# Kernel tuning notes

Hardware: AMD Instinct MI355X
Metric: run time of the kernel (lower is better)

## Reference

```python
import jax, jax.numpy as jnp
import numpy as np

H = 512      # hidden_size
R = 47       # response_size
TR = 2       # treat_size
B = 128
T = 512


def _uniform(key, shape, k):
    return jax.random.uniform(key, shape, jnp.float32, -k, k)


def setup_inputs() -> dict:
    key = jax.random.key(0)
    ks = jax.random.split(key, 20)
    kinit = 1.0 / np.sqrt(H)
    inp = {
        "x_r": jax.random.normal(ks[0], (B, T, R), jnp.float32),
        "x_t": jax.random.normal(ks[1], (B, T, TR), jnp.float32),
        # r_rnn: 2-layer LSTM, input size R+TR=49 (torch gate order i,f,g,o)
        "r_Wih0": _uniform(ks[2], (4 * H, R + TR), kinit),
        "r_Whh0": _uniform(ks[3], (4 * H, H), kinit),
        "r_b0": _uniform(ks[4], (4 * H,), kinit),  # b_ih + b_hh fused
        "r_Wih1": _uniform(ks[5], (4 * H, H), kinit),
        "r_Whh1": _uniform(ks[6], (4 * H, H), kinit),
        "r_b1": _uniform(ks[7], (4 * H,), kinit),
        # t_rnn: 2-layer LSTM, input size 2*R+TR=96
        "t_Wih0": _uniform(ks[8], (4 * H, 2 * R + TR), kinit),
        "t_Whh0": _uniform(ks[9], (4 * H, H), kinit),
        "t_b0": _uniform(ks[10], (4 * H,), kinit),
        "t_Wih1": _uniform(ks[11], (4 * H, H), kinit),
        "t_Whh1": _uniform(ks[12], (4 * H, H), kinit),
        "t_b1": _uniform(ks[13], (4 * H,), kinit),
        # output linears
        "Wr": _uniform(ks[14], (R, H), kinit),
        "br": _uniform(ks[15], (R,), kinit),
        "Wt": _uniform(ks[16], (TR, H), kinit),
        "bt": _uniform(ks[17], (TR,), kinit),
    }
    return inp


def _lstm_cell(x, h, c, Wih, Whh, b):
    gates = x @ Wih.T + h @ Whh.T + b          # [B, 4H]
    i, f, g, o = jnp.split(gates, 4, axis=-1)
    c = jax.nn.sigmoid(f) * c + jax.nn.sigmoid(i) * jnp.tanh(g)
    h = jax.nn.sigmoid(o) * jnp.tanh(c)
    return h, c


def reference(x_r, x_t, r_Wih0, r_Whh0, r_b0, r_Wih1, r_Whh1, r_b1,
              t_Wih0, t_Whh0, t_b0, t_Wih1, t_Whh1, t_b1, Wr, br, Wt, bt):
    b = x_r.shape[0]
    z = jnp.zeros((b, H), x_r.dtype)
    carry0 = (z, z, z, z, z, z, z, z)  # (h,c) for 2 layers of r_rnn and t_rnn

    def step(carry, rt):
        hr0, cr0, hr1, cr1, ht0, ct0, ht1, ct1 = carry
        r, t = rt
        r_input = jnp.concatenate([r, t], axis=-1)          # [B, 49]
        hr0, cr0 = _lstm_cell(r_input, hr0, cr0, r_Wih0, r_Whh0, r_b0)
        hr1, cr1 = _lstm_cell(hr0, hr1, cr1, r_Wih1, r_Whh1, r_b1)
        r_out = hr1 @ Wr.T + br                             # [B, 47]
        t_input = jnp.concatenate([r_input, r_out], axis=-1)  # [B, 96]
        ht0, ct0 = _lstm_cell(t_input, ht0, ct0, t_Wih0, t_Whh0, t_b0)
        ht1, ct1 = _lstm_cell(ht0, ht1, ct1, t_Wih1, t_Whh1, t_b1)
        t_out = ht1 @ Wt.T + bt                             # [B, 2]
        return (hr0, cr0, hr1, cr1, ht0, ct0, ht1, ct1), (r_out, t_out)

    xs = (jnp.swapaxes(x_r, 0, 1), jnp.swapaxes(x_t, 0, 1))  # time-major [T,B,.]
    _, (r_seq, t_seq) = jax.lax.scan(step, carry0, xs)
    # back to batch-first, like the module's final permute(1,0,2)
    return jnp.swapaxes(r_seq, 0, 1), jnp.swapaxes(t_seq, 0, 1)
```

## Files before the change

kernel.cpp:

```cpp
#include <hip/hip_runtime.h>


typedef _Float16 half_t;
typedef _Float16 half8 __attribute__((ext_vector_type(8)));
typedef float floatx4 __attribute__((ext_vector_type(4)));
typedef unsigned long long ull_t;

#define OFF_W0 0
#define OFF_W1 131072
#define OFF_W2 1179648
#define OFF_W3 2228224
#define OFF_W4 3276800
#define OFF_W5 3407872
#define OFF_W6 3538944
#define OFF_W7 4587520
#define OFF_W8 5636096
#define OFF_W9 6684672
#define OFF_W10 6709248
#define W_TOTAL 6717440
#define H_BASE  6717440
#define RO_BASE 7241728
#define HALF_TOTAL 7258112
#define STATE_BYTE_OFF (H_BASE * 2)
#define C_BYTE_OFF (HALF_TOTAL * 2)
#define BAR_BYTE_OFF 15564800
#define X16_BYTE_OFF (BAR_BYTE_OFF + 4096)
#define WS_NEED_X16 ((unsigned long long)X16_BYTE_OFF + 8388608ull)
#define STATE_BYTES (X16_BYTE_OFF - STATE_BYTE_OFF)

#define NBLK 256
#define TOUT_BASE (128 * 512 * 47)

__device__ __forceinline__ floatx4 mfma16(half8 a, half8 b, floatx4 c) {
  return __builtin_amdgcn_mfma_f32_16x16x32_f16(a, b, c, 0, 0, 0);
}
__device__ __forceinline__ float fast_sig(float x) {
  x = fminf(fmaxf(x, -30.f), 30.f);
  float e = __expf(-x);
  return __builtin_amdgcn_rcpf(1.f + e);
}
__device__ __forceinline__ float fast_tanh(float x) {
  x = fminf(fmaxf(x, -15.f), 15.f);
  float e = __expf(-2.f * x);
  return (1.f - e) * __builtin_amdgcn_rcpf(1.f + e);
}

template <int N>
__device__ __forceinline__ void coh_stage(half8 (&bb)[N], const half_t* p) {
#pragma unroll
  for (int ks = 0; ks < N; ++ks)
    asm volatile("global_load_dwordx4 %0, %1, off sc0 sc1"
                 : "=v"(bb[ks]) : "v"(p + ks * 32));
}
__device__ __forceinline__ void drain_vm() {
  asm volatile("s_waitcnt vmcnt(0)" ::: "memory");
  __builtin_amdgcn_sched_barrier(0);
}
__device__ __forceinline__ void store_h4_coh(half_t* p, half_t h0, half_t h1,
                                             half_t h2, half_t h3) {
  union { ull_t u; _Float16 h[4]; } x;
  x.h[0] = h0; x.h[1] = h1; x.h[2] = h2; x.h[3] = h3;
  __hip_atomic_store((ull_t*)p, x.u, __ATOMIC_RELAXED,
                     __HIP_MEMORY_SCOPE_AGENT);
}
template <int PACE>
__device__ __forceinline__ void poll_llc(const unsigned* p, unsigned target) {
  for (;;) {
    unsigned v;
    asm volatile("global_load_dword %0, %1, off sc0 sc1\ns_waitcnt vmcnt(0)"
                 : "=v"(v) : "v"(p));
    if (v >= target) return;
    __builtin_amdgcn_s_sleep(PACE);
  }
}

__device__ __forceinline__ void slab_issue(half8 (&tmp)[4],
                                           const half_t* __restrict__ src,
                                           int tid) {
#pragma unroll
  for (int j = 0; j < 4; ++j) {
    const int u = tid + j * 256;
    asm volatile("global_load_dwordx4 %0, %1, off sc0 sc1"
                 : "=v"(tmp[j]) : "v"(src + (u >> 6) * 512 + (u & 63) * 8));
  }
}
__device__ __forceinline__ void slab_write(char* base, const half8 (&tmp)[4],
                                           int tid) {
#pragma unroll
  for (int j = 0; j < 4; ++j) {
    const int u = tid + j * 256;
    const int row = u >> 6, seg = u & 63;
    *(half8*)(base + row * 1024 + ((seg * 16) ^ ((row & 7) << 4))) = tmp[j];
  }
}

template <int NT, int NSEG, int LDW>
__device__ __forceinline__ void gemm_lb(const half_t* __restrict__ W,
                                        const int* wrow, const char* ldsb,
                                        int lk, int q, int l15,
                                        floatx4 (&acc)[NT]) {
  const int bbase = l15 * 1024;
  const int bxor = (l15 & 7) << 4;
#pragma unroll
  for (int ks = 0; ks < NSEG; ++ks) {
    const int kb = ks * 32 + lk;
    half8 b = *(const half8*)(ldsb + bbase + ((q * 16 + ks * 64) ^ bxor));
#pragma unroll
    for (int n = 0; n < NT; ++n) {
      half8 a = *(const half8*)(W + (long)(wrow[n] + l15) * LDW + kb);
      acc[n] = mfma16(a, b, acc[n]);
    }
  }
}

template <int NT, int NSEG, int LDW>
__device__ __forceinline__ void gemm_regB(const half_t* __restrict__ W,
                                          const int* wrow,
                                          const half8 (&bb)[NSEG], int lk,
                                          int l15, floatx4 (&acc)[NT]) {
#pragma unroll
  for (int ks = 0; ks < NSEG; ++ks) {
    const int kb = ks * 32 + lk;
#pragma unroll
    for (int n = 0; n < NT; ++n) {
      half8 a = *(const half8*)(W + (long)(wrow[n] + l15) * LDW + kb);
      acc[n] = mfma16(a, bb[ks], acc[n]);
    }
  }
}

__device__ __forceinline__ void gemm_x16(const half_t* __restrict__ W,
                                         const int* wrow,
                                         const half_t* __restrict__ xb, int lk,
                                         int l15, floatx4 (&acc)[4]) {
#pragma unroll
  for (int ks = 0; ks < 2; ++ks) {
    const int kb = ks * 32 + lk;
    half8 b = *(const half8*)(xb + kb);
#pragma unroll
    for (int n = 0; n < 4; ++n) {
      half8 a = *(const half8*)(W + (long)(wrow[n] + l15) * 64 + kb);
      acc[n] = mfma16(a, b, acc[n]);
    }
  }
}
__device__ __forceinline__ void gemm_xf(const float* __restrict__ xr,
                                        const float* __restrict__ xt, int t,
                                        int batch, const half_t* __restrict__ W,
                                        const int* wrow, int lk, int l15,
                                        floatx4 (&acc)[4]) {
#pragma unroll
  for (int ks = 0; ks < 2; ++ks) {
    const int kb = ks * 32 + lk;
    half8 b;
    const long base = (long)batch * 512 + t;
#pragma unroll
    for (int j = 0; j < 8; ++j) {
      const int kk = kb + j;
      float f = 0.f;
      if (kk < 47) f = xr[base * 47 + kk];
      else if (kk < 49) f = xt[base * 2 + (kk - 47)];
      b[j] = (half_t)f;
    }
#pragma unroll
    for (int n = 0; n < 4; ++n) {
      half8 a = *(const half8*)(W + (long)(wrow[n] + l15) * 64 + kb);
      acc[n] = mfma16(a, b, acc[n]);
    }
  }
}

__device__ __forceinline__ void lstm_epi_reg(floatx4 (&acc)[4],
                                             const float* __restrict__ bias,
                                             floatx4& creg,
                                             half_t* __restrict__ hdst,
                                             int batch, int hcol0) {
  const floatx4 bI = *(const floatx4*)(bias + hcol0);
  const floatx4 bF = *(const floatx4*)(bias + 512 + hcol0);
  const floatx4 bG = *(const floatx4*)(bias + 1024 + hcol0);
  const floatx4 bO = *(const floatx4*)(bias + 1536 + hcol0);
  const int off = batch * 512 + hcol0;
  half_t hn[4];
#pragma unroll
  for (int r = 0; r < 4; ++r) {
    const float gi = acc[0][r] + bI[r];
    const float gf = acc[1][r] + bF[r];
    const float gg = acc[2][r] + bG[r];
    const float go = acc[3][r] + bO[r];
    creg[r] = fast_sig(gf) * creg[r] + fast_sig(gi) * fast_tanh(gg);
    hn[r] = (half_t)(fast_sig(go) * fast_tanh(creg[r]));
  }
  store_h4_coh(hdst + off, hn[0], hn[1], hn[2], hn[3]);
}

__global__ __launch_bounds__(256, 1) void adrnn_persist(
    const float* __restrict__ xr, const float* __restrict__ xt,
    const float* __restrict__ b_r0, const float* __restrict__ b_r1,
    const float* __restrict__ b_t0, const float* __restrict__ b_t1,
    const float* __restrict__ brv, const float* __restrict__ btv,
    half_t* __restrict__ w16, float* __restrict__ cbase,
    float* __restrict__ out, unsigned* bar, const half_t* __restrict__ x16,
    int use_x16) {
  __shared__ half8 lds_v[2048];
  char* lds0 = (char*)lds_v;
  char* lds1 = lds0 + 16384;

  const int bid = blockIdx.x;
  const int tid = threadIdx.x;
  const int lane = tid & 63;
  const int w = tid >> 6;
  const int l15 = lane & 15;
  const int q = lane >> 4;
  const int lk = q * 8;
  half_t* H = w16 + H_BASE;
  half_t* RO = w16 + RO_BASE;
#define HB(cell, p) (H + (((cell)*2 + (p)) << 16))

  const int stage = (bid & 7) >> 1;
  const int hgHi = bid & 1;
  const int rr = bid >> 3;
  const int hgLo = rr >> 3;
  const int bg = rr & 7;
  const int hg = hgHi * 4 + hgLo;
  const int c0w = hg * 64 + w * 16;
  const int b0 = bg * 16;
  const int batch = b0 + l15;
  const int hcol0 = c0w + q * 4;
  const int sd = (stage == 0) ? 0 : (stage == 1) ? 1 : (stage == 2) ? 3 : 4;
  int wrow[4] = {c0w, 512 + c0w, 1024 + c0w, 1536 + c0w};
  const int flat = (hg * 8 + bg) * 4 + w;
  const bool is_spare = (stage == 0 && hg < 2 && flat < 32);

  unsigned* larr = bar + (bid & 7) * 32;
  unsigned* garr = bar + 256;
  unsigned* lgen = bar + 288 + (bid & 7) * 32;

  floatx4 creg = {0.f, 0.f, 0.f, 0.f};

  for (int k = 0; k < 517; ++k) {
    const int par = k & 1, pq = par ^ 1;
    const int t = k - sd;
    const bool valid = (t >= 0 && t < 512);

    if (valid) {
      half8 s0[4], s1[4];
      if (stage == 0) {
        slab_issue(s0, HB(0, pq) + b0 * 512, tid);
        drain_vm();
        slab_write(lds0, s0, tid);
      } else if (stage == 1) {
        slab_issue(s0, HB(0, pq) + b0 * 512, tid);
        slab_issue(s1, HB(1, pq) + b0 * 512, tid);
        drain_vm();
        slab_write(lds0, s0, tid);
        slab_write(lds1, s1, tid);
      } else if (stage == 2) {
        slab_issue(s0, HB(2, pq) + b0 * 512, tid);
        drain_vm();
        slab_write(lds0, s0, tid);
      } else {
        slab_issue(s0, HB(2, pq) + b0 * 512, tid);
        slab_issue(s1, HB(3, pq) + b0 * 512, tid);
        drain_vm();
        slab_write(lds0, s0, tid);
        slab_write(lds1, s1, tid);
      }
    }
    __syncthreads();

    if (valid) {
      floatx4 acc[4] = {};
      if (stage == 0) {
        if (use_x16)
          gemm_x16(w16 + OFF_W0, wrow, x16 + (long)t * 8192 + batch * 64, lk, l15, acc);
        else
          gemm_xf(xr, xt, t, batch, w16 + OFF_W0, wrow, lk, l15, acc);
        gemm_lb<4, 16, 512>(w16 + OFF_W1, wrow, lds0, lk, q, l15, acc);
        lstm_epi_reg(acc, b_r0, creg, HB(0, par), batch, hcol0);
      } else if (stage == 1) {
        gemm_lb<4, 16, 512>(w16 + OFF_W2, wrow, lds0, lk, q, l15, acc);
        gemm_lb<4, 16, 512>(w16 + OFF_W3, wrow, lds1, lk, q, l15, acc);
        lstm_epi_reg(acc, b_r1, creg, HB(1, par), batch, hcol0);
      } else if (stage == 2) {
        half8 bro[2];
        coh_stage<2>(bro, RO + pq * 8192 + batch * 64 + lk);
        drain_vm();
        if (use_x16)
          gemm_x16(w16 + OFF_W4, wrow, x16 + (long)t * 8192 + batch * 64, lk, l15, acc);
        else
          gemm_xf(xr, xt, t, batch, w16 + OFF_W4, wrow, lk, l15, acc);
        gemm_regB<4, 2, 64>(w16 + OFF_W5, wrow, bro, lk, l15, acc);
        gemm_lb<4, 16, 512>(w16 + OFF_W6, wrow, lds0, lk, q, l15, acc);
        lstm_epi_reg(acc, b_t0, creg, HB(2, par), batch, hcol0);
      } else {
        gemm_lb<4, 16, 512>(w16 + OFF_W7, wrow, lds0, lk, q, l15, acc);
        gemm_lb<4, 16, 512>(w16 + OFF_W8, wrow, lds1, lk, q, l15, acc);
        lstm_epi_reg(acc, b_t1, creg, HB(3, par), batch, hcol0);
      }
    }

    if (is_spare) {
      if (flat < 24) {
        const int tr = k - 2;
        if (tr >= 0 && tr < 512) {
          const int n = flat >> 3, btl = flat & 7;
          const int rb = btl * 16 + l15;
          half8 bs[16];
          coh_stage<16>(bs, HB(1, pq) + rb * 512 + lk);
          drain_vm();
          int wr1[1] = {n * 16};
          floatx4 accr[1] = {};
          gemm_regB<1, 16, 512>(w16 + OFF_W9, wr1, bs, lk, l15, accr);
          const int wc0 = n * 16 + q * 4;
          half_t ro4[4];
#pragma unroll
          for (int r = 0; r < 4; ++r) {
            const int wc = wc0 + r;
            float v = 0.f;
            if (wc < 47) {
              v = accr[0][r] + brv[wc];
              out[((long)rb * 512 + tr) * 47 + wc] = v;
            }
            ro4[r] = (half_t)v;
          }
          store_h4_coh(RO + par * 8192 + rb * 64 + wc0, ro4[0], ro4[1], ro4[2], ro4[3]);
        }
      } else {
        const int tt = k - 5;
        if (tt >= 0 && tt < 512) {
          const int btl = flat - 24;
          const int rb = btl * 16 + l15;
          half8 bs[16];
          coh_stage<16>(bs, HB(3, pq) + rb * 512 + lk);
          drain_vm();
          int wt1[1] = {0};
          floatx4 accw[1] = {};
          gemm_regB<1, 16, 512>(w16 + OFF_W10, wt1, bs, lk, l15, accw);
          if (q == 0) {
#pragma unroll
            for (int r = 0; r < 2; ++r)
              out[TOUT_BASE + ((long)rb * 512 + tt) * 2 + r] = accw[0][r] + btv[r];
          }
        }
      }
    }

    asm volatile("s_waitcnt vmcnt(0)" ::: "memory");
    __syncthreads();
    if (tid == 0) {
      const unsigned ku = (unsigned)k + 1u;
      (void)__hip_atomic_fetch_add(larr, 1u, __ATOMIC_RELAXED,
                                   __HIP_MEMORY_SCOPE_AGENT);
      if (bid < 8) {
        poll_llc<1>(larr, 32u * ku);
        (void)__hip_atomic_fetch_add(garr, 1u, __ATOMIC_RELAXED,
                                     __HIP_MEMORY_SCOPE_AGENT);
        poll_llc<1>(garr, 8u * ku);
        (void)__hip_atomic_fetch_add(lgen, 1u, __ATOMIC_RELAXED,
                                     __HIP_MEMORY_SCOPE_AGENT);
      } else {
        poll_llc<3>(lgen, ku);
      }
    }
    __syncthreads();
    asm volatile("" ::: "memory");
  }
#undef HB
}

__global__ __launch_bounds__(256) void conv_w(
    const float* __restrict__ rWih0, const float* __restrict__ rWhh0,
    const float* __restrict__ rWih1, const float* __restrict__ rWhh1,
    const float* __restrict__ tWih0, const float* __restrict__ tWhh0,
    const float* __restrict__ tWih1, const float* __restrict__ tWhh1,
    const float* __restrict__ Wr, const float* __restrict__ Wt,
    half_t* __restrict__ w16) {
  const int idx = blockIdx.x * 256 + threadIdx.x;
  if (idx >= W_TOTAL) return;
  float v = 0.f;
  if (idx < OFF_W1) {
    int n = idx >> 6, kk = idx & 63;
    if (kk < 49) v = rWih0[n * 49 + kk];
  } else if (idx < OFF_W2) {
    int r = idx - OFF_W1; v = rWhh0[r];
  } else if (idx < OFF_W3) {
    int r = idx - OFF_W2; v = rWih1[r];
  } else if (idx < OFF_W4) {
    int r = idx - OFF_W3; v = rWhh1[r];
  } else if (idx < OFF_W5) {
    int r = idx - OFF_W4; int n = r >> 6, kk = r & 63;
    if (kk < 49) v = tWih0[n * 96 + kk];
  } else if (idx < OFF_W6) {
    int r = idx - OFF_W5; int n = r >> 6, kk = r & 63;
    if (kk < 47) v = tWih0[n * 96 + 49 + kk];
  } else if (idx < OFF_W7) {
    int r = idx - OFF_W6; v = tWhh0[r];
  } else if (idx < OFF_W8) {
    int r = idx - OFF_W7; v = tWih1[r];
  } else if (idx < OFF_W9) {
    int r = idx - OFF_W8; v = tWhh1[r];
  } else if (idx < OFF_W10) {
    int r = idx - OFF_W9; int n = r >> 9, kk = r & 511;
    if (n < 47) v = Wr[n * 512 + kk];
  } else {
    int r = idx - OFF_W10; int n = r >> 9, kk = r & 511;
    if (n < 2) v = Wt[n * 512 + kk];
  }
  w16[idx] = (half_t)v;
}

__global__ __launch_bounds__(256) void conv_x(const float* __restrict__ xr,
                                              const float* __restrict__ xt,
                                              half_t* __restrict__ x16) {
  const int idx = blockIdx.x * 256 + threadIdx.x;
  if (idx >= 512 * 128 * 64) return;
  const int kk = idx & 63;
  const int row = (idx >> 6) & 127;
  const int t = idx >> 13;
  float v = 0.f;
  if (kk < 47) v = xr[(row * 512 + t) * 47 + kk];
  else if (kk < 49) v = xt[(row * 512 + t) * 2 + (kk - 47)];
  x16[idx] = (half_t)v;
}

extern "C" void kernel_launch(void* const* d_in, const int* in_sizes, int n_in,
                              void* d_out, int out_size, void* d_ws,
                              size_t ws_size, hipStream_t stream) {
  const float* xr = (const float*)d_in[0];
  const float* xt = (const float*)d_in[1];
  const float* rWih0 = (const float*)d_in[2];
  const float* rWhh0 = (const float*)d_in[3];
  const float* r_b0 = (const float*)d_in[4];
  const float* rWih1 = (const float*)d_in[5];
  const float* rWhh1 = (const float*)d_in[6];
  const float* r_b1 = (const float*)d_in[7];
  const float* tWih0 = (const float*)d_in[8];
  const float* tWhh0 = (const float*)d_in[9];
  const float* t_b0 = (const float*)d_in[10];
  const float* tWih1 = (const float*)d_in[11];
  const float* tWhh1 = (const float*)d_in[12];
  const float* t_b1 = (const float*)d_in[13];
  const float* Wr = (const float*)d_in[14];
  const float* br = (const float*)d_in[15];
  const float* Wt = (const float*)d_in[16];
  const float* bt = (const float*)d_in[17];

  half_t* w16 = (half_t*)d_ws;
  float* cbase = (float*)((char*)d_ws + C_BYTE_OFF);
  unsigned* bar = (unsigned*)((char*)d_ws + BAR_BYTE_OFF);
  half_t* x16 = (half_t*)((char*)d_ws + X16_BYTE_OFF);
  float* out = (float*)d_out;
  int use_x16 = (ws_size >= WS_NEED_X16) ? 1 : 0;

  (void)hipMemsetAsync((char*)d_ws + STATE_BYTE_OFF, 0, STATE_BYTES, stream);

  conv_w<<<(W_TOTAL + 255) / 256, 256, 0, stream>>>(
      rWih0, rWhh0, rWih1, rWhh1, tWih0, tWhh0, tWih1, tWhh1, Wr, Wt, w16);
  if (use_x16)
    conv_x<<<(512 * 128 * 64) / 256, 256, 0, stream>>>(xr, xt, x16);

  adrnn_persist<<<NBLK, 256, 0, stream>>>(xr, xt, r_b0, r_b1, t_b0, t_b1, br,
                                          bt, w16, cbase, out, bar, x16,
                                          use_x16);
}
```

Baseline: 9.246 ms.

## Replace global grid barrier with per-stage producer/consumer counters and 4-slot buffers

Replaces the per-step two-level global barrier across all 256 blocks with point-to-point counters: each stage polls only the write counters of the stages it consumes and the read counters of its consumers, using 4-deep rotating hidden-state buffers so producers can run ahead. The r_out and t_out output projections move from dedicated spare warps into stage-1 and stage-3 blocks, reusing the hidden state already staged in LDS. The goal is to cut global synchronisation latency and let pipeline stages overlap. In exchange it adds more atomic polling per step, grows the workspace for the extra buffers, and is more complex to get right.

```diff
diff --git a/kernel.cpp b/kernel.cpp
--- a/kernel.cpp
+++ b/kernel.cpp
@@ -19,12 +19,11 @@
 #define OFF_W10 6709248
 #define W_TOTAL 6717440
 #define H_BASE  6717440
-#define RO_BASE 7241728
-#define HALF_TOTAL 7258112
+#define RO_BASE 7766016
+#define HALF_TOTAL 7798784
 #define STATE_BYTE_OFF (H_BASE * 2)
-#define C_BYTE_OFF (HALF_TOTAL * 2)
-#define BAR_BYTE_OFF 15564800
-#define X16_BYTE_OFF (BAR_BYTE_OFF + 4096)
+#define BAR_BYTE_OFF (HALF_TOTAL * 2)
+#define X16_BYTE_OFF (BAR_BYTE_OFF + 16384)
 #define WS_NEED_X16 ((unsigned long long)X16_BYTE_OFF + 8388608ull)
 #define STATE_BYTES (X16_BYTE_OFF - STATE_BYTE_OFF)
 
@@ -46,7 +45,7 @@
 }
 
 template <int N>
-__device__ __forceinline__ void coh_stage(half8 (&bb)[N], const half_t* p) {
+__device__ __forceinline__ void burst_g(half8 (&bb)[N], const half_t* p) {
 #pragma unroll
   for (int ks = 0; ks < N; ++ks)
     asm volatile("global_load_dwordx4 %0, %1, off sc0 sc1"
@@ -56,22 +55,21 @@
   asm volatile("s_waitcnt vmcnt(0)" ::: "memory");
   __builtin_amdgcn_sched_barrier(0);
 }
-__device__ __forceinline__ void store_h4_coh(half_t* p, half_t h0, half_t h1,
-                                             half_t h2, half_t h3) {
-  union { ull_t u; _Float16 h[4]; } x;
-  x.h[0] = h0; x.h[1] = h1; x.h[2] = h2; x.h[3] = h3;
-  __hip_atomic_store((ull_t*)p, x.u, __ATOMIC_RELAXED,
-                     __HIP_MEMORY_SCOPE_AGENT);
-}
-template <int PACE>
+__device__ __forceinline__ void store_h4_coh(half_t* p, ull_t v) {
+  __hip_atomic_store((ull_t*)p, v, __ATOMIC_RELAXED, __HIP_MEMORY_SCOPE_AGENT);
+}
 __device__ __forceinline__ void poll_llc(const unsigned* p, unsigned target) {
   for (;;) {
     unsigned v;
     asm volatile("global_load_dword %0, %1, off sc0 sc1\ns_waitcnt vmcnt(0)"
                  : "=v"(v) : "v"(p));
     if (v >= target) return;
-    __builtin_amdgcn_s_sleep(PACE);
-  }
+    __builtin_amdgcn_s_sleep(1);
+  }
+}
+__device__ __forceinline__ void cnt_add(unsigned* p) {
+  (void)__hip_atomic_fetch_add(p, 1u, __ATOMIC_RELAXED,
+                               __HIP_MEMORY_SCOPE_AGENT);
 }
 
 __device__ __forceinline__ void slab_issue(half8 (&tmp)[4],
@@ -112,7 +110,6 @@
     }
   }
 }
-
 template <int NT, int NSEG, int LDW>
 __device__ __forceinline__ void gemm_regB(const half_t* __restrict__ W,
                                           const int* wrow,
@@ -128,7 +125,6 @@
     }
   }
 }
-
 __device__ __forceinline__ void gemm_x16(const half_t* __restrict__ W,
                                          const int* wrow,
                                          const half_t* __restrict__ xb, int lk,
@@ -180,7 +176,7 @@
   const floatx4 bG = *(const floatx4*)(bias + 1024 + hcol0);
   const floatx4 bO = *(const floatx4*)(bias + 1536 + hcol0);
   const int off = batch * 512 + hcol0;
-  half_t hn[4];
+  union { ull_t u; _Float16 h[4]; } pk;
 #pragma unroll
   for (int r = 0; r < 4; ++r) {
     const float gi = acc[0][r] + bI[r];
@@ -188,9 +184,9 @@
     const float gg = acc[2][r] + bG[r];
     const float go = acc[3][r] + bO[r];
     creg[r] = fast_sig(gf) * creg[r] + fast_sig(gi) * fast_tanh(gg);
-    hn[r] = (half_t)(fast_sig(go) * fast_tanh(creg[r]));
-  }
-  store_h4_coh(hdst + off, hn[0], hn[1], hn[2], hn[3]);
+    pk.h[r] = (half_t)(fast_sig(go) * fast_tanh(creg[r]));
+  }
+  store_h4_coh(hdst + off, pk.u);
 }
 
 __global__ __launch_bounds__(256, 1) void adrnn_persist(
@@ -214,7 +210,7 @@
   const int lk = q * 8;
   half_t* H = w16 + H_BASE;
   half_t* RO = w16 + RO_BASE;
-#define HB(cell, p) (H + (((cell)*2 + (p)) << 16))
+#define HB(cell, s) (H + (((cell)*4 + (s)) << 16))
 
   const int stage = (bid & 7) >> 1;
   const int hgHi = bid & 1;
@@ -228,45 +224,88 @@
   const int hcol0 = c0w + q * 4;
   const int sd = (stage == 0) ? 0 : (stage == 1) ? 1 : (stage == 2) ? 3 : 4;
   int wrow[4] = {c0w, 512 + c0w, 1024 + c0w, 1536 + c0w};
-  const int flat = (hg * 8 + bg) * 4 + w;
-  const bool is_spare = (stage == 0 && hg < 2 && flat < 32);
-
-  unsigned* larr = bar + (bid & 7) * 32;
-  unsigned* garr = bar + 256;
-  unsigned* lgen = bar + 288 + (bid & 7) * 32;
+
+#define WRH(c, b) (bar + ((c)*8 + (b)) * 32)
+#define RDA(c, b) (bar + 1024 + ((c)*8 + (b)) * 32)
+#define RDB(c, b) (bar + 2048 + ((c)*8 + (b)) * 32)
+#define WRRO(b)   (bar + 3072 + (b)*32)
+#define RDRO(b)   (bar + 3328 + (b)*32)
 
   floatx4 creg = {0.f, 0.f, 0.f, 0.f};
 
   for (int k = 0; k < 517; ++k) {
-    const int par = k & 1, pq = par ^ 1;
+    const int rs = (k - 1) & 3;
+    const int wsl = k & 3;
     const int t = k - sd;
     const bool valid = (t >= 0 && t < 512);
-
-    if (valid) {
+    const unsigned ku = (unsigned)k;
+
+    if (tid == 0) {
+      if (k > 0) {
+        if (stage == 0) {
+          poll_llc(WRH(0, bg), 8u * ku);
+        } else if (stage == 1) {
+          poll_llc(WRH(0, bg), 8u * ku);
+          poll_llc(WRH(1, bg), 8u * ku);
+        } else if (stage == 2) {
+          poll_llc(WRH(2, bg), 8u * ku);
+          poll_llc(WRRO(bg), ku);
+        } else {
+          poll_llc(WRH(2, bg), 8u * ku);
+          poll_llc(WRH(3, bg), 8u * ku);
+        }
+      }
+      if (k >= 3) {
+        const unsigned kw = ku - 2u;
+        if (stage == 0) {
+          poll_llc(RDA(0, bg), 8u * kw);
+          poll_llc(RDB(0, bg), 8u * kw);
+        } else if (stage == 1) {
+          poll_llc(RDA(1, bg), 8u * kw);
+          if (hg == 0) poll_llc(RDRO(bg), 8u * kw);
+        } else if (stage == 2) {
+          poll_llc(RDA(2, bg), 8u * kw);
+          poll_llc(RDB(2, bg), 8u * kw);
+        } else {
+          poll_llc(RDA(3, bg), 8u * kw);
+        }
+      }
+    }
+    __syncthreads();
+
+    half8 bro[2];
+    {
       half8 s0[4], s1[4];
       if (stage == 0) {
-        slab_issue(s0, HB(0, pq) + b0 * 512, tid);
+        slab_issue(s0, HB(0, rs) + b0 * 512, tid);
         drain_vm();
         slab_write(lds0, s0, tid);
       } else if (stage == 1) {
-        slab_issue(s0, HB(0, pq) + b0 * 512, tid);
-        slab_issue(s1, HB(1, pq) + b0 * 512, tid);
+        slab_issue(s0, HB(0, rs) + b0 * 512, tid);
+        slab_issue(s1, HB(1, rs) + b0 * 512, tid);
         drain_vm();
         slab_write(lds0, s0, tid);
         slab_write(lds1, s1, tid);
       } else if (stage == 2) {
-        slab_issue(s0, HB(2, pq) + b0 * 512, tid);
+        slab_issue(s0, HB(2, rs) + b0 * 512, tid);
+        burst_g<2>(bro, RO + rs * 8192 + batch * 64 + lk);
         drain_vm();
         slab_write(lds0, s0, tid);
       } else {
-        slab_issue(s0, HB(2, pq) + b0 * 512, tid);
-        slab_issue(s1, HB(3, pq) + b0 * 512, tid);
+        slab_issue(s0, HB(2, rs) + b0 * 512, tid);
+        slab_issue(s1, HB(3, rs) + b0 * 512, tid);
         drain_vm();
         slab_write(lds0, s0, tid);
         slab_write(lds1, s1, tid);
       }
     }
     __syncthreads();
+    if (tid == 0) {
+      if (stage == 0) cnt_add(RDA(0, bg));
+      else if (stage == 1) { cnt_add(RDB(0, bg)); cnt_add(RDA(1, bg)); }
+      else if (stage == 2) { cnt_add(RDA(2, bg)); cnt_add(RDRO(bg)); }
+      else { cnt_add(RDB(2, bg)); cnt_add(RDA(3, bg)); }
+    }
 
     if (valid) {
       floatx4 acc[4] = {};
@@ -276,96 +315,76 @@
         else
           gemm_xf(xr, xt, t, batch, w16 + OFF_W0, wrow, lk, l15, acc);
         gemm_lb<4, 16, 512>(w16 + OFF_W1, wrow, lds0, lk, q, l15, acc);
-        lstm_epi_reg(acc, b_r0, creg, HB(0, par), batch, hcol0);
+        lstm_epi_reg(acc, b_r0, creg, HB(0, wsl), batch, hcol0);
       } else if (stage == 1) {
         gemm_lb<4, 16, 512>(w16 + OFF_W2, wrow, lds0, lk, q, l15, acc);
         gemm_lb<4, 16, 512>(w16 + OFF_W3, wrow, lds1, lk, q, l15, acc);
-        lstm_epi_reg(acc, b_r1, creg, HB(1, par), batch, hcol0);
+        lstm_epi_reg(acc, b_r1, creg, HB(1, wsl), batch, hcol0);
       } else if (stage == 2) {
-        half8 bro[2];
-        coh_stage<2>(bro, RO + pq * 8192 + batch * 64 + lk);
-        drain_vm();
         if (use_x16)
           gemm_x16(w16 + OFF_W4, wrow, x16 + (long)t * 8192 + batch * 64, lk, l15, acc);
         else
           gemm_xf(xr, xt, t, batch, w16 + OFF_W4, wrow, lk, l15, acc);
         gemm_regB<4, 2, 64>(w16 + OFF_W5, wrow, bro, lk, l15, acc);
         gemm_lb<4, 16, 512>(w16 + OFF_W6, wrow, lds0, lk, q, l15, acc);
-        lstm_epi_reg(acc, b_t0, creg, HB(2, par), batch, hcol0);
+        lstm_epi_reg(acc, b_t0, creg, HB(2, wsl), batch, hcol0);
       } else {
         gemm_lb<4, 16, 512>(w16 + OFF_W7, wrow, lds0, lk, q, l15, acc);
         gemm_lb<4, 16, 512>(w16 + OFF_W8, wrow, lds1, lk, q, l15, acc);
-        lstm_epi_reg(acc, b_t1, creg, HB(3, par), batch, hcol0);
-      }
-    }
-
-    if (is_spare) {
-      if (flat < 24) {
-        const int tr = k - 2;
-        if (tr >= 0 && tr < 512) {
-          const int n = flat >> 3, btl = flat & 7;
-          const int rb = btl * 16 + l15;
-          half8 bs[16];
-          coh_stage<16>(bs, HB(1, pq) + rb * 512 + lk);
-          drain_vm();
-          int wr1[1] = {n * 16};
-          floatx4 accr[1] = {};
-          gemm_regB<1, 16, 512>(w16 + OFF_W9, wr1, bs, lk, l15, accr);
-          const int wc0 = n * 16 + q * 4;
-          half_t ro4[4];
-#pragma unroll
-          for (int r = 0; r < 4; ++r) {
-            const int wc = wc0 + r;
-            float v = 0.f;
-            if (wc < 47) {
-              v = accr[0][r] + brv[wc];
-              out[((long)rb * 512 + tr) * 47 + wc] = v;
-            }
-            ro4[r] = (half_t)v;
+        lstm_epi_reg(acc, b_t1, creg, HB(3, wsl), batch, hcol0);
+      }
+    }
+
+    if (stage == 1 && hg == 0 && w < 3) {
+      const int tro = k - 2;
+      if (tro >= 0 && tro < 512) {
+        int wr1[1] = {w * 16};
+        floatx4 accr[1] = {};
+        gemm_lb<1, 16, 512>(w16 + OFF_W9, wr1, lds1, lk, q, l15, accr);
+        const int rb = b0 + l15;
+        const int wc0 = w * 16 + q * 4;
+        union { ull_t u2; _Float16 h[4]; } rp;
+#pragma unroll
+        for (int r = 0; r < 4; ++r) {
+          const int wc = wc0 + r;
+          float v = 0.f;
+          if (wc < 47) {
+            v = accr[0][r] + brv[wc];
+            out[((long)rb * 512 + tro) * 47 + wc] = v;
           }
-          store_h4_coh(RO + par * 8192 + rb * 64 + wc0, ro4[0], ro4[1], ro4[2], ro4[3]);
+          rp.h[r] = (half_t)v;
         }
-      } else {
-        const int tt = k - 5;
-        if (tt >= 0 && tt < 512) {
-          const int btl = flat - 24;
-          const int rb = btl * 16 + l15;
-          half8 bs[16];
-          coh_stage<16>(bs, HB(3, pq) + rb * 512 + lk);
-          drain_vm();
-          int wt1[1] = {0};
-          floatx4 accw[1] = {};
-          gemm_regB<1, 16, 512>(w16 + OFF_W10, wt1, bs, lk, l15, accw);
-          if (q == 0) {
-#pragma unroll
-            for (int r = 0; r < 2; ++r)
-              out[TOUT_BASE + ((long)rb * 512 + tt) * 2 + r] = accw[0][r] + btv[r];
-          }
+        store_h4_coh(RO + wsl * 8192 + rb * 64 + wc0, rp.u2);
+      }
+    }
+    if (stage == 3 && hg == 0 && w == 0) {
+      const int tto = k - 5;
+      if (tto >= 0 && tto < 512) {
+        int wt1[1] = {0};
+        floatx4 accw[1] = {};
+        gemm_lb<1, 16, 512>(w16 + OFF_W10, wt1, lds1, lk, q, l15, accw);
+        if (q == 0) {
+          const int rb = b0 + l15;
+#pragma unroll
+          for (int r = 0; r < 2; ++r)
+            out[TOUT_BASE + ((long)rb * 512 + tto) * 2 + r] = accw[0][r] + btv[r];
         }
       }
     }
 
-    asm volatile("s_waitcnt vmcnt(0)" ::: "memory");
+    drain_vm();
     __syncthreads();
     if (tid == 0) {
-      const unsigned ku = (unsigned)k + 1u;
-      (void)__hip_atomic_fetch_add(larr, 1u, __ATOMIC_RELAXED,
-                                   __HIP_MEMORY_SCOPE_AGENT);
-      if (bid < 8) {
-        poll_llc<1>(larr, 32u * ku);
-        (void)__hip_atomic_fetch_add(garr, 1u, __ATOMIC_RELAXED,
-                                     __HIP_MEMORY_SCOPE_AGENT);
-        poll_llc<1>(garr, 8u * ku);
-        (void)__hip_atomic_fetch_add(lgen, 1u, __ATOMIC_RELAXED,
-                                     __HIP_MEMORY_SCOPE_AGENT);
-      } else {
-        poll_llc<3>(lgen, ku);
-      }
-    }
-    __syncthreads();
-    asm volatile("" ::: "memory");
+      cnt_add(WRH(stage, bg));
+      if (stage == 1 && hg == 0) cnt_add(WRRO(bg));
+    }
   }
 #undef HB
+#undef WRH
+#undef RDA
+#undef RDB
+#undef WRRO
+#undef RDRO
 }
 
 __global__ __launch_bounds__(256) void conv_w(
@@ -446,7 +465,7 @@
   const float* bt = (const float*)d_in[17];
 
   half_t* w16 = (half_t*)d_ws;
-  float* cbase = (float*)((char*)d_ws + C_BYTE_OFF);
+  float* cbase = nullptr;
   unsigned* bar = (unsigned*)((char*)d_ws + BAR_BYTE_OFF);
   half_t* x16 = (half_t*)((char*)d_ws + X16_BYTE_OFF);
   float* out = (float*)d_out;
```

After: 10.20 ms. 10.3% more time.

## Split K across two wave groups per block and prefetch weight fragments

Applied to the files above, without the earlier changes.

Doubles the block to 512 threads and has each half of the waves compute half of the K reduction for the same gate tile, then reduces the partial accumulators through LDS before the LSTM epilogue. The gemm_lb loop also gets software prefetching of the next weight fragment. The aim is to shorten each recurrent step's serial MFMA chain and hide weight-load latency. In exchange it adds two extra __syncthreads and LDS traffic per step, and uses more registers per wave.

```diff
diff --git a/kernel.cpp b/kernel.cpp
--- a/kernel.cpp
+++ b/kernel.cpp
@@ -56,12 +56,8 @@
   asm volatile("s_waitcnt vmcnt(0)" ::: "memory");
   __builtin_amdgcn_sched_barrier(0);
 }
-__device__ __forceinline__ void store_h4_coh(half_t* p, half_t h0, half_t h1,
-                                             half_t h2, half_t h3) {
-  union { ull_t u; _Float16 h[4]; } x;
-  x.h[0] = h0; x.h[1] = h1; x.h[2] = h2; x.h[3] = h3;
-  __hip_atomic_store((ull_t*)p, x.u, __ATOMIC_RELAXED,
-                     __HIP_MEMORY_SCOPE_AGENT);
+__device__ __forceinline__ void store_h4_coh(half_t* p, ull_t v) {
+  __hip_atomic_store((ull_t*)p, v, __ATOMIC_RELAXED, __HIP_MEMORY_SCOPE_AGENT);
 }
 template <int PACE>
 __device__ __forceinline__ void poll_llc(const unsigned* p, unsigned target) {
@@ -74,21 +70,21 @@
   }
 }
 
-__device__ __forceinline__ void slab_issue(half8 (&tmp)[4],
-                                           const half_t* __restrict__ src,
-                                           int tid) {
-#pragma unroll
-  for (int j = 0; j < 4; ++j) {
-    const int u = tid + j * 256;
+__device__ __forceinline__ void slab_issue2(half8 (&tmp)[2],
+                                            const half_t* __restrict__ src,
+                                            int tid) {
+#pragma unroll
+  for (int j = 0; j < 2; ++j) {
+    const int u = tid + j * 512;
     asm volatile("global_load_dwordx4 %0, %1, off sc0 sc1"
                  : "=v"(tmp[j]) : "v"(src + (u >> 6) * 512 + (u & 63) * 8));
   }
 }
-__device__ __forceinline__ void slab_write(char* base, const half8 (&tmp)[4],
-                                           int tid) {
-#pragma unroll
-  for (int j = 0; j < 4; ++j) {
-    const int u = tid + j * 256;
+__device__ __forceinline__ void slab_write2(char* base, const half8 (&tmp)[2],
+                                            int tid) {
+#pragma unroll
+  for (int j = 0; j < 2; ++j) {
+    const int u = tid + j * 512;
     const int row = u >> 6, seg = u & 63;
     *(half8*)(base + row * 1024 + ((seg * 16) ^ ((row & 7) << 4))) = tmp[j];
   }
@@ -97,22 +93,42 @@
 template <int NT, int NSEG, int LDW>
 __device__ __forceinline__ void gemm_lb(const half_t* __restrict__ W,
                                         const int* wrow, const char* ldsb,
-                                        int lk, int q, int l15,
+                                        int ks0, int lk, int q, int l15,
                                         floatx4 (&acc)[NT]) {
   const int bbase = l15 * 1024;
   const int bxor = (l15 & 7) << 4;
-#pragma unroll
-  for (int ks = 0; ks < NSEG; ++ks) {
-    const int kb = ks * 32 + lk;
+  half8 a_cur[NT], a_nxt[NT];
+#pragma unroll
+  for (int n = 0; n < NT; ++n)
+    a_cur[n] = *(const half8*)(W + (long)(wrow[n] + l15) * LDW + ks0 * 32 + lk);
+#pragma unroll
+  for (int ksl = 0; ksl < NSEG; ++ksl) {
+    const int ks = ks0 + ksl;
+    if (ksl + 1 < NSEG) {
+      const int kb2 = (ks + 1) * 32 + lk;
+#pragma unroll
+      for (int n = 0; n < NT; ++n)
+        a_nxt[n] = *(const half8*)(W + (long)(wrow[n] + l15) * LDW + kb2);
+    }
     half8 b = *(const half8*)(ldsb + bbase + ((q * 16 + ks * 64) ^ bxor));
 #pragma unroll
-    for (int n = 0; n < NT; ++n) {
-      half8 a = *(const half8*)(W + (long)(wrow[n] + l15) * LDW + kb);
-      acc[n] = mfma16(a, b, acc[n]);
-    }
-  }
-}
-
+    for (int n = 0; n < NT; ++n) acc[n] = mfma16(a_cur[n], b, acc[n]);
+#pragma unroll
+    for (int n = 0; n < NT; ++n) a_cur[n] = a_nxt[n];
+  }
+}
+template <int NT>
+__device__ __forceinline__ void gemm_seg(const half_t* __restrict__ W,
+                                         const int* wrow, half8 b, int ks,
+                                         int LDW, int lk, int l15,
+                                         floatx4 (&acc)[NT]) {
+  const int kb = ks * 32 + lk;
+#pragma unroll
+  for (int n = 0; n < NT; ++n) {
+    half8 a = *(const half8*)(W + (long)(wrow[n] + l15) * LDW + kb);
+    acc[n] = mfma16(a, b, acc[n]);
+  }
+}
 template <int NT, int NSEG, int LDW>
 __device__ __forceinline__ void gemm_regB(const half_t* __restrict__ W,
                                           const int* wrow,
@@ -129,45 +145,21 @@
   }
 }
 
-__device__ __forceinline__ void gemm_x16(const half_t* __restrict__ W,
-                                         const int* wrow,
-                                         const half_t* __restrict__ xb, int lk,
-                                         int l15, floatx4 (&acc)[4]) {
-#pragma unroll
-  for (int ks = 0; ks < 2; ++ks) {
-    const int kb = ks * 32 + lk;
-    half8 b = *(const half8*)(xb + kb);
-#pragma unroll
-    for (int n = 0; n < 4; ++n) {
-      half8 a = *(const half8*)(W + (long)(wrow[n] + l15) * 64 + kb);
-      acc[n] = mfma16(a, b, acc[n]);
-    }
-  }
-}
-__device__ __forceinline__ void gemm_xf(const float* __restrict__ xr,
-                                        const float* __restrict__ xt, int t,
-                                        int batch, const half_t* __restrict__ W,
-                                        const int* wrow, int lk, int l15,
-                                        floatx4 (&acc)[4]) {
-#pragma unroll
-  for (int ks = 0; ks < 2; ++ks) {
-    const int kb = ks * 32 + lk;
-    half8 b;
-    const long base = (long)batch * 512 + t;
-#pragma unroll
-    for (int j = 0; j < 8; ++j) {
-      const int kk = kb + j;
-      float f = 0.f;
-      if (kk < 47) f = xr[base * 47 + kk];
-      else if (kk < 49) f = xt[base * 2 + (kk - 47)];
-      b[j] = (half_t)f;
-    }
-#pragma unroll
-    for (int n = 0; n < 4; ++n) {
-      half8 a = *(const half8*)(W + (long)(wrow[n] + l15) * 64 + kb);
-      acc[n] = mfma16(a, b, acc[n]);
-    }
-  }
+__device__ __forceinline__ half8 build_bx1(const float* __restrict__ xr,
+                                           const float* __restrict__ xt, int t,
+                                           int batch, int ks, int lk) {
+  half8 b;
+  const long base = (long)batch * 512 + t;
+  const int kb = ks * 32 + lk;
+#pragma unroll
+  for (int j = 0; j < 8; ++j) {
+    const int kk = kb + j;
+    float f = 0.f;
+    if (kk < 47) f = xr[base * 47 + kk];
+    else if (kk < 49) f = xt[base * 2 + (kk - 47)];
+    b[j] = (half_t)f;
+  }
+  return b;
 }
 
 __device__ __forceinline__ void lstm_epi_reg(floatx4 (&acc)[4],
@@ -180,7 +172,7 @@
   const floatx4 bG = *(const floatx4*)(bias + 1024 + hcol0);
   const floatx4 bO = *(const floatx4*)(bias + 1536 + hcol0);
   const int off = batch * 512 + hcol0;
-  half_t hn[4];
+  union { ull_t u; _Float16 h[4]; } pk;
 #pragma unroll
   for (int r = 0; r < 4; ++r) {
     const float gi = acc[0][r] + bI[r];
@@ -188,12 +180,12 @@
     const float gg = acc[2][r] + bG[r];
     const float go = acc[3][r] + bO[r];
     creg[r] = fast_sig(gf) * creg[r] + fast_sig(gi) * fast_tanh(gg);
-    hn[r] = (half_t)(fast_sig(go) * fast_tanh(creg[r]));
-  }
-  store_h4_coh(hdst + off, hn[0], hn[1], hn[2], hn[3]);
-}
-
-__global__ __launch_bounds__(256, 1) void adrnn_persist(
+    pk.h[r] = (half_t)(fast_sig(go) * fast_tanh(creg[r]));
+  }
+  store_h4_coh(hdst + off, pk.u);
+}
+
+__global__ __launch_bounds__(512, 1) void adrnn_persist(
     const float* __restrict__ xr, const float* __restrict__ xt,
     const float* __restrict__ b_r0, const float* __restrict__ b_r1,
     const float* __restrict__ b_t0, const float* __restrict__ b_t1,
@@ -208,7 +200,9 @@
   const int bid = blockIdx.x;
   const int tid = threadIdx.x;
   const int lane = tid & 63;
-  const int w = tid >> 6;
+  const int w8 = tid >> 6;
+  const int hw = w8 & 3;
+  const int kh = w8 >> 2;
   const int l15 = lane & 15;
   const int q = lane >> 4;
   const int lk = q * 8;
@@ -222,14 +216,15 @@
   const int hgLo = rr >> 3;
   const int bg = rr & 7;
   const int hg = hgHi * 4 + hgLo;
-  const int c0w = hg * 64 + w * 16;
+  const int c0w = hg * 64 + hw * 16;
   const int b0 = bg * 16;
   const int batch = b0 + l15;
   const int hcol0 = c0w + q * 4;
   const int sd = (stage == 0) ? 0 : (stage == 1) ? 1 : (stage == 2) ? 3 : 4;
   int wrow[4] = {c0w, 512 + c0w, 1024 + c0w, 1536 + c0w};
-  const int flat = (hg * 8 + bg) * 4 + w;
-  const bool is_spare = (stage == 0 && hg < 2 && flat < 32);
+  const int ks0 = kh * 8;
+  const int flat = (hg * 8 + bg) * 4 + hw;
+  const bool is_spare = (stage == 0 && hg < 2 && flat < 32 && kh == 0);
 
   unsigned* larr = bar + (bid & 7) * 32;
   unsigned* garr = bar + 256;
@@ -243,60 +238,78 @@
     const bool valid = (t >= 0 && t < 512);
 
     if (valid) {
-      half8 s0[4], s1[4];
+      half8 s0[2], s1[2];
       if (stage == 0) {
-        slab_issue(s0, HB(0, pq) + b0 * 512, tid);
+        slab_issue2(s0, HB(0, pq) + b0 * 512, tid);
         drain_vm();
-        slab_write(lds0, s0, tid);
+        slab_write2(lds0, s0, tid);
       } else if (stage == 1) {
-        slab_issue(s0, HB(0, pq) + b0 * 512, tid);
-        slab_issue(s1, HB(1, pq) + b0 * 512, tid);
+        slab_issue2(s0, HB(0, pq) + b0 * 512, tid);
+        slab_issue2(s1, HB(1, pq) + b0 * 512, tid);
         drain_vm();
-        slab_write(lds0, s0, tid);
-        slab_write(lds1, s1, tid);
+        slab_write2(lds0, s0, tid);
+        slab_write2(lds1, s1, tid);
       } else if (stage == 2) {
-        slab_issue(s0, HB(2, pq) + b0 * 512, tid);
+        slab_issue2(s0, HB(2, pq) + b0 * 512, tid);
         drain_vm();
-        slab_write(lds0, s0, tid);
+        slab_write2(lds0, s0, tid);
       } else {
-        slab_issue(s0, HB(2, pq) + b0 * 512, tid);
-        slab_issue(s1, HB(3, pq) + b0 * 512, tid);
+        slab_issue2(s0, HB(2, pq) + b0 * 512, tid);
+        slab_issue2(s1, HB(3, pq) + b0 * 512, tid);
         drain_vm();
-        slab_write(lds0, s0, tid);
-        slab_write(lds1, s1, tid);
+        slab_write2(lds0, s0, tid);
+        slab_write2(lds1, s1, tid);
       }
     }
     __syncthreads();
 
+    floatx4 acc[4] = {};
     if (valid) {
-      floatx4 acc[4] = {};
       if (stage == 0) {
+        half8 bx;
         if (use_x16)
-          gemm_x16(w16 + OFF_W0, wrow, x16 + (long)t * 8192 + batch * 64, lk, l15, acc);
+          bx = *(const half8*)(x16 + (long)t * 8192 + batch * 64 + kh * 32 + lk);
         else
-          gemm_xf(xr, xt, t, batch, w16 + OFF_W0, wrow, lk, l15, acc);
-        gemm_lb<4, 16, 512>(w16 + OFF_W1, wrow, lds0, lk, q, l15, acc);
-        lstm_epi_reg(acc, b_r0, creg, HB(0, par), batch, hcol0);
+          bx = build_bx1(xr, xt, t, batch, kh, lk);
+        gemm_seg<4>(w16 + OFF_W0, wrow, bx, kh, 64, lk, l15, acc);
+        gemm_lb<4, 8, 512>(w16 + OFF_W1, wrow, lds0, ks0, lk, q, l15, acc);
       } else if (stage == 1) {
-        gemm_lb<4, 16, 512>(w16 + OFF_W2, wrow, lds0, lk, q, l15, acc);
-        gemm_lb<4, 16, 512>(w16 + OFF_W3, wrow, lds1, lk, q, l15, acc);
-        lstm_epi_reg(acc, b_r1, creg, HB(1, par), batch, hcol0);
+        gemm_lb<4, 8, 512>(w16 + OFF_W2, wrow, lds0, ks0, lk, q, l15, acc);
+        gemm_lb<4, 8, 512>(w16 + OFF_W3, wrow, lds1, ks0, lk, q, l15, acc);
       } else if (stage == 2) {
-        half8 bro[2];
-        coh_stage<2>(bro, RO + pq * 8192 + batch * 64 + lk);
+        half8 bro;
+        asm volatile("global_load_dwordx4 %0, %1, off sc0 sc1"
+                     : "=v"(bro)
+                     : "v"(RO + pq * 8192 + batch * 64 + kh * 32 + lk));
+        half8 bx;
+        if (use_x16)
+          bx = *(const half8*)(x16 + (long)t * 8192 + batch * 64 + kh * 32 + lk);
+        else
+          bx = build_bx1(xr, xt, t, batch, kh, lk);
+        gemm_seg<4>(w16 + OFF_W4, wrow, bx, kh, 64, lk, l15, acc);
         drain_vm();
-        if (use_x16)
-          gemm_x16(w16 + OFF_W4, wrow, x16 + (long)t * 8192 + batch * 64, lk, l15, acc);
-        else
-          gemm_xf(xr, xt, t, batch, w16 + OFF_W4, wrow, lk, l15, acc);
-        gemm_regB<4, 2, 64>(w16 + OFF_W5, wrow, bro, lk, l15, acc);
-        gemm_lb<4, 16, 512>(w16 + OFF_W6, wrow, lds0, lk, q, l15, acc);
-        lstm_epi_reg(acc, b_t0, creg, HB(2, par), batch, hcol0);
+        gemm_seg<4>(w16 + OFF_W5, wrow, bro, kh, 64, lk, l15, acc);
+        gemm_lb<4, 8, 512>(w16 + OFF_W6, wrow, lds0, ks0, lk, q, l15, acc);
       } else {
-        gemm_lb<4, 16, 512>(w16 + OFF_W7, wrow, lds0, lk, q, l15, acc);
-        gemm_lb<4, 16, 512>(w16 + OFF_W8, wrow, lds1, lk, q, l15, acc);
-        lstm_epi_reg(acc, b_t1, creg, HB(3, par), batch, hcol0);
+        gemm_lb<4, 8, 512>(w16 + OFF_W7, wrow, lds0, ks0, lk, q, l15, acc);
+        gemm_lb<4, 8, 512>(w16 + OFF_W8, wrow, lds1, ks0, lk, q, l15, acc);
       }
+    }
+    __syncthreads();
+
+    if (valid && kh == 1) {
+#pragma unroll
+      for (int n = 0; n < 4; ++n)
+        *(floatx4*)(lds0 + hw * 4096 + lane * 64 + n * 16) = acc[n];
+    }
+    __syncthreads();
+    if (valid && kh == 0) {
+#pragma unroll
+      for (int n = 0; n < 4; ++n)
+        acc[n] += *(const floatx4*)(lds0 + hw * 4096 + lane * 64 + n * 16);
+      const float* bias = (stage == 0) ? b_r0 : (stage == 1) ? b_r1
+                         : (stage == 2) ? b_t0 : b_t1;
+      lstm_epi_reg(acc, bias, creg, HB(stage, par), batch, hcol0);
     }
 
     if (is_spare) {
@@ -312,7 +325,7 @@
           floatx4 accr[1] = {};
           gemm_regB<1, 16, 512>(w16 + OFF_W9, wr1, bs, lk, l15, accr);
           const int wc0 = n * 16 + q * 4;
-          half_t ro4[4];
+          union { ull_t u2; _Float16 h[4]; } rp;
 #pragma unroll
           for (int r = 0; r < 4; ++r) {
             const int wc = wc0 + r;
@@ -321,9 +334,9 @@
               v = accr[0][r] + brv[wc];
               out[((long)rb * 512 + tr) * 47 + wc] = v;
             }
-            ro4[r] = (half_t)v;
+            rp.h[r] = (half_t)v;
           }
-          store_h4_coh(RO + par * 8192 + rb * 64 + wc0, ro4[0], ro4[1], ro4[2], ro4[3]);
+          store_h4_coh(RO + par * 8192 + rb * 64 + wc0, rp.u2);
         }
       } else {
         const int tt = k - 5;
@@ -446,7 +459,7 @@
   const float* bt = (const float*)d_in[17];
 
   half_t* w16 = (half_t*)d_ws;
-  float* cbase = (float*)((char*)d_ws + C_BYTE_OFF);
+  float* cbase = nullptr;
   unsigned* bar = (unsigned*)((char*)d_ws + BAR_BYTE_OFF);
   half_t* x16 = (half_t*)((char*)d_ws + X16_BYTE_OFF);
   float* out = (float*)d_out;
@@ -459,7 +472,7 @@
   if (use_x16)
     conv_x<<<(512 * 128 * 64) / 256, 256, 0, stream>>>(xr, xt, x16);
 
-  adrnn_persist<<<NBLK, 256, 0, stream>>>(xr, xt, r_b0, r_b1, t_b0, t_b1, br,
+  adrnn_persist<<<NBLK, 512, 0, stream>>>(xr, xt, r_b0, r_b1, t_b0, t_b1, br,
                                           bt, w16, cbase, out, bar, x16,
                                           use_x16);
 }
```

Result: slower. 14.02 ms (+51.6%).
